# Kernel tuning notes

Hardware: AMD Instinct MI355X
Metric: run time of the kernel (lower is better)

The kernel has to match this reference:

```python
import jax, jax.numpy as jnp
import numpy as np

LAMB = 1.0
EPS = 1e-16


def setup_inputs() -> dict:
    key = jax.random.key(0)
    kx, km = jax.random.split(key)
    N, D, K = 262144, 128, 64
    x = jax.random.normal(kx, (N, D), dtype=jnp.float32)
    m = jax.random.normal(km, (K, D), dtype=jnp.float32)
    m = m / jnp.linalg.norm(m, axis=1, keepdims=True)  # unit-norm rows like __init__
    return {"x": x, "m": m}


def _entropy(p):
    # replicate torch.where clamping
    p = jnp.where(p <= 0, EPS, p)
    p = jnp.where(p >= 1, 1.0 - EPS, p)
    return -jnp.sum(p * jnp.log(p), axis=-1)


def _p(x, m):
    d2 = (jnp.sum(x * x, axis=-1, keepdims=True)
          - 2.0 * x @ m.T
          + jnp.sum(m * m, axis=-1))  # [N, K]
    return jax.nn.softmax(-d2, axis=-1)


def reference(x, m):
    p = _p(x, m)                      # [N, K]
    intra = jnp.mean(_entropy(p))     # scalar
    mu = jnp.mean(m, axis=0)          # [D]
    p_inter = _p(mu[None, :], m)[0]   # [K]
    inter = _entropy(p_inter)
    total = intra - LAMB * inter
    return (total, intra, inter)
```

## Files before the change

kernel.cpp:

```cpp
#include <hip/hip_runtime.h>
#include <hip/hip_bf16.h>

#define D 128
#define K 64

typedef __attribute__((ext_vector_type(8))) short short8;
typedef __attribute__((ext_vector_type(4))) float f32x4;

__device__ inline short f2bf(float f) {
  union { float f; unsigned u; } v; v.f = f;
  unsigned u = v.u;
  return (short)((u + 0x7fffu + ((u >> 16) & 1u)) >> 16);
}

__device__ inline unsigned pk2(float a, float b) {
  union { __hip_bfloat162 h; unsigned u; } c;
  c.h = __float22bfloat162_rn(make_float2(a, b));
  return c.u;
}

template<int CTRL>
__device__ inline float dpp_add(float v) {
  int r = __builtin_amdgcn_update_dpp(0, __float_as_int(v), CTRL, 0xf, 0xf, true);
  return v + __int_as_float(r);
}
__device__ inline float row16_allsum(float v) {
  v = dpp_add<0x121>(v);
  v = dpp_add<0x122>(v);
  v = dpp_add<0x124>(v);
  v = dpp_add<0x128>(v);
  return v;
}

__global__ void prep_kernel(const float* __restrict__ m, float* ws) {
  const int j = blockIdx.x;
  const int t = threadIdx.x;
  float a0 = m[j * D + t * 2];
  float a1 = m[j * D + t * 2 + 1];
  short* mb = (short*)(ws + 128);
  mb[j * D + t * 2]     = f2bf(2.0f * a0);
  mb[j * D + t * 2 + 1] = f2bf(2.0f * a1);
  float s = a0 * a0 + a1 * a1;
  for (int off = 1; off < 64; off <<= 1) s += __shfl_xor(s, off, 64);
  if (t == 0) ws[16 + j] = s;
  if (j == 0 && t < 16) ws[t] = 0.0f;
}

__launch_bounds__(256)
__global__ void main_kernel(const float* __restrict__ x, float* ws) {
  const float* mnorm = ws + 16;
  const short* mb = (const short*)(ws + 128);
  const int tid  = threadIdx.x;
  const int lane = tid & 63;
  const int wv   = tid >> 6;
  const int lid  = lane & 15;
  const int quad = lane >> 4;

  const int wave = blockIdx.x * 4 + wv;
  const int cnt  = 5 + (wave < 1024 ? 1 : 0);
  const int base = wave * 5 + (wave < 1024 ? wave : 1024);

  f32x4 v[8];
  {
    const float* xb = x + (size_t)(base * 16 + lid) * D + quad * 8;
#pragma unroll
    for (int kk = 0; kk < 4; ++kk) {
      v[2 * kk]     = *(const f32x4*)(xb + kk * 32);
      v[2 * kk + 1] = *(const f32x4*)(xb + kk * 32 + 4);
    }
  }

  short8 bfr[4][4];
  float mn[4];
#pragma unroll
  for (int jt = 0; jt < 4; ++jt) {
    mn[jt] = mnorm[jt * 16 + lid];
#pragma unroll
    for (int kk = 0; kk < 4; ++kk)
      bfr[jt][kk] = *(const short8*)(mb + (jt * 16 + lid) * D + kk * 32 + quad * 8);
  }

  float hacc = 0.f;

  for (int it = 0; it < cnt; ++it) {
    const bool more = (it + 1 < cnt);
    const float* xn = x + (size_t)((base + it + 1) * 16 + lid) * D + quad * 8;

    f32x4 acc[4];
#pragma unroll
    for (int jt = 0; jt < 4; ++jt) acc[jt] = (f32x4){0.f, 0.f, 0.f, 0.f};

#pragma unroll
    for (int kk = 0; kk < 4; ++kk) {
      f32x4 v0 = v[2 * kk], v1 = v[2 * kk + 1];
      union { short8 s; unsigned u[4]; } av;
      av.u[0] = pk2(v0[0], v0[1]);
      av.u[1] = pk2(v0[2], v0[3]);
      av.u[2] = pk2(v1[0], v1[1]);
      av.u[3] = pk2(v1[2], v1[3]);
      if (more) {
        v[2 * kk]     = *(const f32x4*)(xn + kk * 32);
        v[2 * kk + 1] = *(const f32x4*)(xn + kk * 32 + 4);
      }
#pragma unroll
      for (int jt = 0; jt < 4; ++jt)
        acc[jt] = __builtin_amdgcn_mfma_f32_16x16x32_bf16(av.s, bfr[jt][kk], acc[jt], 0, 0, 0);
    }

#pragma unroll
    for (int r = 0; r < 4; ++r) {
      float s0 = acc[0][r] - mn[0];
      float s1 = acc[1][r] - mn[1];
      float s2 = acc[2][r] - mn[2];
      float s3 = acc[3][r] - mn[3];
      float e0 = __expf(s0), e1 = __expf(s1), e2 = __expf(s2), e3 = __expf(s3);
      float S0 = (e0 + e1) + (e2 + e3);
      float S1 = fmaf(s0, e0, fmaf(s1, e1, fmaf(s2, e2, s3 * e3)));
      S0 = row16_allsum(S0);
      S1 = row16_allsum(S1);
      float H = __logf(S0) - S1 / S0;
      if (lid == 0) hacc += H;
    }
  }

  for (int off = 1; off < 64; off <<= 1) hacc += __shfl_xor(hacc, off, 64);
  __shared__ float red[4];
  if (lane == 0) red[wv] = hacc;
  __syncthreads();
  if (tid == 0) atomicAdd(ws, red[0] + red[1] + red[2] + red[3]);
}

__global__ void final_kernel(const float* __restrict__ m, const float* ws, float* out, int nRows) {
  __shared__ float mu[D];
  int lane = threadIdx.x;
  for (int d = lane; d < D; d += 64) {
    float s = 0.f;
    for (int j = 0; j < K; ++j) s += m[j * D + d];
    mu[d] = s * (1.0f / K);
  }
  __syncthreads();
  const float* mr = m + lane * D;
  float dot = 0.f;
  for (int d = 0; d < D; ++d) dot += mu[d] * mr[d];
  float s = 2.f * dot - ws[16 + lane];
  float t = s - 20.f;
  float e = __expf(t);
  float S0 = e, S1 = t * e;
  for (int off = 1; off < 64; off <<= 1) {
    S0 += __shfl_xor(S0, off, 64);
    S1 += __shfl_xor(S1, off, 64);
  }
  float inter = __logf(S0) - S1 / S0;
  if (lane == 0) {
    float intra = ws[0] / (float)nRows;
    out[0] = intra - inter;
    out[1] = intra;
    out[2] = inter;
  }
}

extern "C" void kernel_launch(void* const* d_in, const int* in_sizes, int n_in,
                              void* d_out, int out_size, void* d_ws, size_t ws_size,
                              hipStream_t stream) {
  const float* x = (const float*)d_in[0];
  const float* m = (const float*)d_in[1];
  float* ws = (float*)d_ws;
  float* out = (float*)d_out;
  const int N = in_sizes[0] / D;

  prep_kernel<<<64, 64, 0, stream>>>(m, ws);

  main_kernel<<<768, 256, 0, stream>>>(x, ws);

  final_kernel<<<1, 64, 0, stream>>>(m, ws, out, N);
}
```

Baseline: 212.8 us.

## Stage x tiles through LDS with coalesced loads and double-buffered prefetch

Measured after the change: 213.9 us. About the same (+0.5%).

```diff
diff --git a/kernel.cpp b/kernel.cpp
--- a/kernel.cpp
+++ b/kernel.cpp
@@ -3,9 +3,11 @@
 
 #define D 128
 #define K 64
+#define MROW 136
 
 typedef __attribute__((ext_vector_type(8))) short short8;
 typedef __attribute__((ext_vector_type(4))) float f32x4;
+typedef __attribute__((ext_vector_type(2))) unsigned uint2v;
 
 __device__ inline short f2bf(float f) {
   union { float f; unsigned u; } v; v.f = f;
@@ -48,6 +50,8 @@
 
 __launch_bounds__(256)
 __global__ void main_kernel(const float* __restrict__ x, float* ws) {
+  __shared__ short msB[64 * MROW];
+  __shared__ short msA[4][16 * MROW];
   const float* mnorm = ws + 16;
   const short* mb = (const short*)(ws + 128);
   const int tid  = threadIdx.x;
@@ -57,54 +61,69 @@
   const int quad = lane >> 4;
 
   const int wave = blockIdx.x * 4 + wv;
-  const int cnt  = 5 + (wave < 1024 ? 1 : 0);
-  const int base = wave * 5 + (wave < 1024 ? wave : 1024);
+  const int base = wave * 4;
 
-  f32x4 v[8];
+  f32x4 v0[8], v1[8];
   {
-    const float* xb = x + (size_t)(base * 16 + lid) * D + quad * 8;
+    const f32x4* t0 = (const f32x4*)(x + (size_t)base * 2048);
+    const f32x4* t1 = t0 + 512;
 #pragma unroll
-    for (int kk = 0; kk < 4; ++kk) {
-      v[2 * kk]     = *(const f32x4*)(xb + kk * 32);
-      v[2 * kk + 1] = *(const f32x4*)(xb + kk * 32 + 4);
-    }
+    for (int j = 0; j < 8; ++j) v0[j] = t0[j * 64 + lane];
+#pragma unroll
+    for (int j = 0; j < 8; ++j) v1[j] = t1[j * 64 + lane];
   }
 
-  short8 bfr[4][4];
+#pragma unroll
+  for (int i = 0; i < 4; ++i) {
+    int g = i * 2048 + tid * 8;
+    int row = g >> 7, col = g & 127;
+    *(short8*)(msB + row * MROW + col) = *(const short8*)(mb + g);
+  }
   float mn[4];
 #pragma unroll
-  for (int jt = 0; jt < 4; ++jt) {
-    mn[jt] = mnorm[jt * 16 + lid];
-#pragma unroll
-    for (int kk = 0; kk < 4; ++kk)
-      bfr[jt][kk] = *(const short8*)(mb + (jt * 16 + lid) * D + kk * 32 + quad * 8);
-  }
+  for (int jt = 0; jt < 4; ++jt) mn[jt] = mnorm[jt * 16 + lid];
+  __syncthreads();
+
+  short* As = msA[wv];
+  const int wrow_hi = lane >> 5;
+  const int wcol = (lane * 4) & 127;
 
   float hacc = 0.f;
 
-  for (int it = 0; it < cnt; ++it) {
-    const bool more = (it + 1 < cnt);
-    const float* xn = x + (size_t)((base + it + 1) * 16 + lid) * D + quad * 8;
+#pragma unroll
+  for (int it = 0; it < 4; ++it) {
+    f32x4* cur = (it & 1) ? v1 : v0;
+
+#pragma unroll
+    for (int j = 0; j < 8; ++j) {
+      f32x4 w = cur[j];
+      uint2v p;
+      p[0] = pk2(w[0], w[1]);
+      p[1] = pk2(w[2], w[3]);
+      *(uint2v*)(As + (j * 2 + wrow_hi) * MROW + wcol) = p;
+    }
+
+    if (it + 2 < 4) {
+      const f32x4* tn = (const f32x4*)(x + (size_t)(base + it + 2) * 2048);
+#pragma unroll
+      for (int j = 0; j < 8; ++j) cur[j] = tn[j * 64 + lane];
+    }
+
+    short8 a[4];
+#pragma unroll
+    for (int kk = 0; kk < 4; ++kk)
+      a[kk] = *(const short8*)(As + lid * MROW + kk * 32 + quad * 8);
 
     f32x4 acc[4];
 #pragma unroll
     for (int jt = 0; jt < 4; ++jt) acc[jt] = (f32x4){0.f, 0.f, 0.f, 0.f};
-
 #pragma unroll
     for (int kk = 0; kk < 4; ++kk) {
-      f32x4 v0 = v[2 * kk], v1 = v[2 * kk + 1];
-      union { short8 s; unsigned u[4]; } av;
-      av.u[0] = pk2(v0[0], v0[1]);
-      av.u[1] = pk2(v0[2], v0[3]);
-      av.u[2] = pk2(v1[0], v1[1]);
-      av.u[3] = pk2(v1[2], v1[3]);
-      if (more) {
-        v[2 * kk]     = *(const f32x4*)(xn + kk * 32);
-        v[2 * kk + 1] = *(const f32x4*)(xn + kk * 32 + 4);
+#pragma unroll
+      for (int jt = 0; jt < 4; ++jt) {
+        short8 b = *(const short8*)(msB + (jt * 16 + lid) * MROW + kk * 32 + quad * 8);
+        acc[jt] = __builtin_amdgcn_mfma_f32_16x16x32_bf16(a[kk], b, acc[jt], 0, 0, 0);
       }
-#pragma unroll
-      for (int jt = 0; jt < 4; ++jt)
-        acc[jt] = __builtin_amdgcn_mfma_f32_16x16x32_bf16(av.s, bfr[jt][kk], acc[jt], 0, 0, 0);
     }
 
 #pragma unroll
@@ -170,7 +189,7 @@
 
   prep_kernel<<<64, 64, 0, stream>>>(m, ws);
 
-  main_kernel<<<768, 256, 0, stream>>>(x, ws);
+  main_kernel<<<1024, 256, 0, stream>>>(x, ws);
 
   final_kernel<<<1, 64, 0, stream>>>(m, ws, out, N);
 }
```
